# Optimization experiments

Hardware: AMD Instinct MI355X
Metric: run time of the kernel (lower is better)

The kernel has to match this reference:

```python
import jax, jax.numpy as jnp
import numpy as np

DIM = 1024
DFF = 4096
LN_EPS = 1e-5


def _layernorm(x, g, b):
    mu = jnp.mean(x, axis=-1, keepdims=True)
    var = jnp.mean((x - mu) ** 2, axis=-1, keepdims=True)
    return (x - mu) * jax.lax.rsqrt(var + LN_EPS) * g + b


def setup_inputs() -> dict:
    key = jax.random.key(0)
    ks = jax.random.split(key, 16)
    B, L, D, F = 4, 2048, DIM, DFF
    return {
        "x": jax.random.normal(ks[0], (B, L, D), dtype=jnp.float32),
        "hidden_real": jax.random.normal(ks[1], (B, D), dtype=jnp.float32),
        "hidden_imag": jax.random.normal(ks[2], (B, D), dtype=jnp.float32),
        # SConvLayer params (real/imag pairs, mirroring torch.view_as_real storage)
        "phazor_init": jax.random.normal(ks[3], (D, 2), dtype=jnp.float32),
        "phazor": jax.random.normal(ks[4], (D, 2), dtype=jnp.float32),
        # fc (gate) linear
        "fc_w": jax.random.normal(ks[5], (D, D), dtype=jnp.float32) / np.sqrt(D),
        "fc_b": jax.random.normal(ks[6], (D,), dtype=jnp.float32) * 0.01,
        # FFN
        "w1": jax.random.normal(ks[7], (F, D), dtype=jnp.float32) / np.sqrt(D),
        "b1": jax.random.normal(ks[8], (F,), dtype=jnp.float32) * 0.01,
        "w2": jax.random.normal(ks[9], (D, F), dtype=jnp.float32) / np.sqrt(F),
        "b2": jax.random.normal(ks[10], (D,), dtype=jnp.float32) * 0.01,
        # shared LayerNorm (used twice in the block with the same params)
        "ln_g": jnp.ones((D,), dtype=jnp.float32),
        "ln_b": jnp.zeros((D,), dtype=jnp.float32),
    }


def reference(x, hidden_real, hidden_imag, phazor_init, phazor,
              fc_w, fc_b, w1, b1, w2, b2, ln_g, ln_b):
    B, L, D = x.shape
    hidden = (hidden_real + 1j * hidden_imag).astype(jnp.complex64)

    x_res = x
    xn = _layernorm(x, ln_g, ln_b)

    # --- SConvLayer ---
    pz = (phazor[:, 0] + 1j * phazor[:, 1]).astype(jnp.complex64)  # [D]
    # magnitude exp(-|z|^2), phase = angle(z)
    p = jnp.exp(-(pz.real ** 2 + pz.imag ** 2)) * jnp.exp(1j * jnp.angle(pz))
    t = jnp.arange(L)
    prog = p[None, :] ** t[:, None]                      # [L, D] complex
    init_c = (phazor_init[:, 0] + 1j * phazor_init[:, 1]).astype(jnp.complex64)
    filt = prog * init_c[None, :]                        # [L, D]
    n2 = 2 * L
    filt_fft = jnp.fft.fft(filt, n=n2, axis=0)           # [2L, D]
    x_fft = jnp.fft.fft(xn.astype(jnp.complex64), n=n2, axis=1)  # [B, 2L, D]
    conv = jnp.fft.ifft(filt_fft[None] * x_fft, axis=1)[:, :L]   # [B, L, D]
    conv_with_past = conv + hidden[:, None, :] * prog[None] * p[None, None, :]
    sx = conv_with_past.real

    # --- gate ---
    y = jax.nn.silu(jnp.einsum('bld,ed->ble', x_res, fc_w) + fc_b)
    x2 = sx * y + x_res

    # --- FFN (same LayerNorm params) ---
    x3 = _layernorm(x2, ln_g, ln_b)
    h = jax.nn.silu(jnp.einsum('bld,fd->blf', x3, w1) + b1)
    out = jnp.einsum('blf,df->bld', h, w2) + b2 + x2
    return out, conv_with_past
```

## Files before the change

kernel.cpp:

```cpp
#include <hip/hip_runtime.h>
#include <hip/hip_bf16.h>

#define D_MODEL 1024
#define D_FF    4096
#define SEQ_LEN 2048
#define NBATCH  4
#define NROWS   (NBATCH*SEQ_LEN)
#define NCHUNK  32
#define CHUNK_L (SEQ_LEN/NCHUNK)
#define LN_EPS  1e-5f

typedef __hip_bfloat16 bf16;
typedef __attribute__((ext_vector_type(8))) short bf16x8;
typedef __attribute__((ext_vector_type(4))) float f32x4;

__device__ __forceinline__ void gload16(const bf16* g, bf16* l) {
    __builtin_amdgcn_global_load_lds(
        (const __attribute__((address_space(1))) void*)g,
        (__attribute__((address_space(3))) void*)l, 16, 0, 0);
}

__global__ void cast4(const float4* __restrict__ in, ushort4* __restrict__ out, int n4) {
    int i = blockIdx.x * blockDim.x + threadIdx.x;
    if (i < n4) {
        float4 v = in[i];
        union { ushort4 u; bf16 b[4]; } cv;
        cv.b[0] = __float2bfloat16(v.x); cv.b[1] = __float2bfloat16(v.y);
        cv.b[2] = __float2bfloat16(v.z); cv.b[3] = __float2bfloat16(v.w);
        out[i] = cv.u;
    }
}

__global__ void compute_pvec(const float* __restrict__ phz, float* __restrict__ pv) {
    int d = blockIdx.x * blockDim.x + threadIdx.x;
    if (d >= D_MODEL) return;
    float re = phz[2*d], im = phz[2*d+1];
    float r2 = re*re + im*im;
    float mag = expf(-r2);
    float pr, pim;
    if (r2 > 0.f) { float inv = mag / sqrtf(r2); pr = re*inv; pim = im*inv; }
    else          { pr = mag; pim = 0.f; }
    float ar = pr, ai = pim;
    #pragma unroll
    for (int i = 0; i < 6; i++) { float nr = ar*ar - ai*ai; float ni = 2.f*ar*ai; ar = nr; ai = ni; }
    pv[d]            = pr;
    pv[D_MODEL+d]    = pim;
    pv[2*D_MODEL+d]  = ar;
    pv[3*D_MODEL+d]  = ai;
}

__global__ __launch_bounds__(256) void ln_fused(const float* __restrict__ x,
                                                const float* __restrict__ g,
                                                const float* __restrict__ bta,
                                                bf16*  __restrict__ outb,
                                                bf16*  __restrict__ rawb)
{
    int row = blockIdx.x;
    int tid = threadIdx.x;
    const float4* xr = (const float4*)(x + (size_t)row * D_MODEL);
    float4 v = xr[tid];
    if (rawb) {
        union { ushort4 u; bf16 b[4]; } cv;
        cv.b[0]=__float2bfloat16(v.x); cv.b[1]=__float2bfloat16(v.y);
        cv.b[2]=__float2bfloat16(v.z); cv.b[3]=__float2bfloat16(v.w);
        ((ushort4*)(rawb + (size_t)row * D_MODEL))[tid] = cv.u;
    }
    float s  = v.x + v.y + v.z + v.w;
    float s2 = v.x*v.x + v.y*v.y + v.z*v.z + v.w*v.w;
    for (int off = 32; off; off >>= 1) { s += __shfl_down(s, off); s2 += __shfl_down(s2, off); }
    __shared__ float red[8];
    int wid = tid >> 6, lane = tid & 63;
    if (lane == 0) { red[wid] = s; red[4+wid] = s2; }
    __syncthreads();
    if (tid == 0) {
        red[0] = red[0]+red[1]+red[2]+red[3];
        red[4] = red[4]+red[5]+red[6]+red[7];
    }
    __syncthreads();
    float mu  = red[0] * (1.f/D_MODEL);
    float var = red[4] * (1.f/D_MODEL) - mu*mu;
    float rstd = rsqrtf(var + LN_EPS);
    float4 gv = ((const float4*)g)[tid];
    float4 bv = ((const float4*)bta)[tid];
    union { ushort4 u; bf16 b[4]; } cv;
    cv.b[0] = __float2bfloat16((v.x-mu)*rstd*gv.x + bv.x);
    cv.b[1] = __float2bfloat16((v.y-mu)*rstd*gv.y + bv.y);
    cv.b[2] = __float2bfloat16((v.z-mu)*rstd*gv.z + bv.z);
    cv.b[3] = __float2bfloat16((v.w-mu)*rstd*gv.w + bv.w);
    ((ushort4*)(outb + (size_t)row * D_MODEL))[tid] = cv.u;
}

__global__ __launch_bounds__(256) void gate_ln(const float* __restrict__ cwp, int cstride,
                                               const bf16*  __restrict__ y,
                                               const float* __restrict__ x,
                                               const float* __restrict__ g,
                                               const float* __restrict__ bta,
                                               bf16*  __restrict__ x2b,
                                               bf16*  __restrict__ x3b)
{
    int row = blockIdx.x;
    int tid = threadIdx.x;
    size_t base = (size_t)row * D_MODEL + tid*4;
    float4 xv = *(const float4*)(x + base);
    union { ushort4 u; bf16 b[4]; } yv;
    yv.u = *(const ushort4*)(y + base);
    float4 cw;
    if (cstride == 1) {
        cw = *(const float4*)(cwp + base);
    } else {
        const float2* cp = (const float2*)cwp + base;
        cw.x = cp[0].x; cw.y = cp[1].x; cw.z = cp[2].x; cw.w = cp[3].x;
    }
    float4 v;
    v.x = cw.x * __bfloat162float(yv.b[0]) + xv.x;
    v.y = cw.y * __bfloat162float(yv.b[1]) + xv.y;
    v.z = cw.z * __bfloat162float(yv.b[2]) + xv.z;
    v.w = cw.w * __bfloat162float(yv.b[3]) + xv.w;
    union { ushort4 u; bf16 b[4]; } c2;
    c2.b[0]=__float2bfloat16(v.x); c2.b[1]=__float2bfloat16(v.y);
    c2.b[2]=__float2bfloat16(v.z); c2.b[3]=__float2bfloat16(v.w);
    *(ushort4*)(x2b + base) = c2.u;

    float s  = v.x + v.y + v.z + v.w;
    float s2 = v.x*v.x + v.y*v.y + v.z*v.z + v.w*v.w;
    for (int off = 32; off; off >>= 1) { s += __shfl_down(s, off); s2 += __shfl_down(s2, off); }
    __shared__ float red[8];
    int wid = tid >> 6, lane = tid & 63;
    if (lane == 0) { red[wid] = s; red[4+wid] = s2; }
    __syncthreads();
    if (tid == 0) {
        red[0] = red[0]+red[1]+red[2]+red[3];
        red[4] = red[4]+red[5]+red[6]+red[7];
    }
    __syncthreads();
    float mu  = red[0] * (1.f/D_MODEL);
    float var = red[4] * (1.f/D_MODEL) - mu*mu;
    float rstd = rsqrtf(var + LN_EPS);
    float4 gv = ((const float4*)g)[tid];
    float4 bv = ((const float4*)bta)[tid];
    union { ushort4 u; bf16 b[4]; } cv;
    cv.b[0] = __float2bfloat16((v.x-mu)*rstd*gv.x + bv.x);
    cv.b[1] = __float2bfloat16((v.y-mu)*rstd*gv.y + bv.y);
    cv.b[2] = __float2bfloat16((v.z-mu)*rstd*gv.z + bv.z);
    cv.b[3] = __float2bfloat16((v.w-mu)*rstd*gv.w + bv.w);
    *(ushort4*)(x3b + base) = cv.u;
}

__global__ __launch_bounds__(256) void scan_pass1(const bf16* __restrict__ xn,
                                                  const float* __restrict__ pv,
                                                  const float* __restrict__ pini,
                                                  float* __restrict__ Sc)
{
    int d = blockIdx.x * 256 + threadIdx.x;
    int c = blockIdx.y, b = blockIdx.z;
    float pr = pv[d], pim = pv[D_MODEL+d];
    float icr = pini[2*d], ici = pini[2*d+1];
    float Sr = 0.f, Si = 0.f;
    const bf16* xp = xn + ((size_t)b*SEQ_LEN + c*CHUNK_L) * D_MODEL + d;
    #pragma unroll 8
    for (int i = 0; i < CHUNK_L; i++) {
        float xv = __bfloat162float(xp[(size_t)i * D_MODEL]);
        float nr = pr*Sr - pim*Si + icr*xv;
        float ni = pr*Si + pim*Sr + ici*xv;
        Sr = nr; Si = ni;
    }
    size_t o = ((size_t)b*NCHUNK + c) * D_MODEL + d;
    Sc[2*o] = Sr; Sc[2*o+1] = Si;
}

__global__ __launch_bounds__(256) void scan_prefix(const float* __restrict__ Sc,
                                                   const float* __restrict__ pv,
                                                   const float* __restrict__ hr,
                                                   const float* __restrict__ hi,
                                                   float* __restrict__ pref)
{
    int d = blockIdx.x * 256 + threadIdx.x;
    int b = blockIdx.y;
    float qr = pv[2*D_MODEL+d], qi = pv[3*D_MODEL+d];
    float Ur = hr[b*D_MODEL+d], Ui = hi[b*D_MODEL+d];
    for (int c = 0; c < NCHUNK; c++) {
        size_t o = ((size_t)b*NCHUNK + c) * D_MODEL + d;
        pref[2*o] = Ur; pref[2*o+1] = Ui;
        float sr = Sc[2*o], si = Sc[2*o+1];
        float nr = qr*Ur - qi*Ui + sr;
        float ni = qr*Ui + qi*Ur + si;
        Ur = nr; Ui = ni;
    }
}

__global__ __launch_bounds__(256) void scan_pass2(const bf16* __restrict__ xn,
                                                  const float* __restrict__ pv,
                                                  const float* __restrict__ pini,
                                                  const float* __restrict__ pref,
                                                  float* __restrict__ cwp,
                                                  int interleaved)
{
    int d = blockIdx.x * 256 + threadIdx.x;
    int c = blockIdx.y, b = blockIdx.z;
    float pr = pv[d], pim = pv[D_MODEL+d];
    float icr = pini[2*d], ici = pini[2*d+1];
    size_t po = ((size_t)b*NCHUNK + c) * D_MODEL + d;
    float Ur = pref[2*po], Ui = pref[2*po+1];
    size_t base = ((size_t)b*SEQ_LEN + c*CHUNK_L) * D_MODEL + d;
    const bf16* xp = xn + base;
    if (interleaved) {
        float2* cp = (float2*)cwp + base;
        #pragma unroll 8
        for (int i = 0; i < CHUNK_L; i++) {
            float xv = __bfloat162float(xp[(size_t)i * D_MODEL]);
            float nr = pr*Ur - pim*Ui + icr*xv;
            float ni = pr*Ui + pim*Ur + ici*xv;
            Ur = nr; Ui = ni;
            cp[(size_t)i * D_MODEL] = make_float2(Ur, Ui);
        }
    } else {
        float* cp = cwp + base;
        #pragma unroll 8
        for (int i = 0; i < CHUNK_L; i++) {
            float xv = __bfloat162float(xp[(size_t)i * D_MODEL]);
            float nr = pr*Ur - pim*Ui + icr*xv;
            float ni = pr*Ui + pim*Ur + ici*xv;
            Ur = nr; Ui = ni;
            cp[(size_t)i * D_MODEL] = Ur;
        }
    }
}

template<int EPI>
__device__ __forceinline__ void epi_store(float v, size_t idx,
                                          const bf16* e0b, float* outf, bf16* outb)
{
    if (EPI == 1) {
        float yv = v / (1.f + __expf(-v));
        outb[idx] = __float2bfloat16(yv);
    } else {
        outf[idx] = v + __bfloat162float(e0b[idx]);
    }
}

#define BM 128
#define BN 128
#define BK 32

template<int EPI>
__global__ __launch_bounds__(256) void gemm_bt(const bf16* __restrict__ A,
                                               const bf16* __restrict__ Bt,
                                               const float* __restrict__ bias,
                                               const bf16* __restrict__ e0b,
                                               float* __restrict__ outf,
                                               bf16*  __restrict__ outb,
                                               int M, int N, int K)
{
    __shared__ __align__(16) bf16 As[3][BM*BK];
    __shared__ __align__(16) bf16 Bs[3][BM*BK];
    int tid = threadIdx.x;
    int m0 = blockIdx.x * BM;
    int n0 = blockIdx.y * BN;

    int wid = tid >> 6, lane = tid & 63;
    int wm = (wid >> 1) * 64, wn = (wid & 1) * 64;
    int lr = lane & 15;
    int lkc = lane >> 4;

    int rl = lane >> 2;
    int cS = (lane & 3) ^ ((rl >> 1) & 3);
    const bf16* gA0 = A  + (size_t)(m0 +      wid*16 + rl) * K + cS*8;
    const bf16* gA1 = A  + (size_t)(m0 + 64 + wid*16 + rl) * K + cS*8;
    const bf16* gB0 = Bt + (size_t)(n0 +      wid*16 + rl) * K + cS*8;
    const bf16* gB1 = Bt + (size_t)(n0 + 64 + wid*16 + rl) * K + cS*8;
    int lo0 = (     wid*16) * BK;
    int lo1 = (64 + wid*16) * BK;

    int keyr = (lr >> 1) & 3;
    int cR = (lkc ^ keyr) * 8;
    int offA[4], offB[4];
    #pragma unroll
    for (int i = 0; i < 4; i++) {
        offA[i] = (wm + i*16 + lr) * BK + cR;
        offB[i] = (wn + i*16 + lr) * BK + cR;
    }

    int nt = K / BK;
    auto stage = [&](int slot, int tile) {
        int k0 = tile * BK;
        gload16(gA0 + k0, &As[slot][lo0]);
        gload16(gA1 + k0, &As[slot][lo1]);
        gload16(gB0 + k0, &Bs[slot][lo0]);
        gload16(gB1 + k0, &Bs[slot][lo1]);
    };
    f32x4 acc[4][4] = {};
    auto compute = [&](int slot) {
        bf16x8 af[4], bfv[4];
        #pragma unroll
        for (int i = 0; i < 4; i++) {
            af[i]  = *(const bf16x8*)&As[slot][offA[i]];
            bfv[i] = *(const bf16x8*)&Bs[slot][offB[i]];
        }
        #pragma unroll
        for (int i = 0; i < 4; i++)
            #pragma unroll
            for (int j = 0; j < 4; j++)
                acc[i][j] = __builtin_amdgcn_mfma_f32_16x16x32_bf16(af[i], bfv[j], acc[i][j], 0, 0, 0);
    };

    stage(0, 0); stage(1, 1); stage(2, 2);

    int s = 0;
    for (int t = 0; t < nt - 3; ++t) {
        asm volatile("s_waitcnt vmcnt(8)" ::: "memory");
        __builtin_amdgcn_s_barrier();
        __builtin_amdgcn_sched_barrier(0);
        compute(s);
        asm volatile("" ::: "memory");
        __builtin_amdgcn_s_barrier();
        stage(s, t + 3);
        s = (s == 2) ? 0 : s + 1;
    }
    asm volatile("s_waitcnt vmcnt(8)" ::: "memory");
    __builtin_amdgcn_s_barrier();
    __builtin_amdgcn_sched_barrier(0);
    compute(s);
    s = (s == 2) ? 0 : s + 1;
    asm volatile("s_waitcnt vmcnt(4)" ::: "memory");
    __builtin_amdgcn_s_barrier();
    __builtin_amdgcn_sched_barrier(0);
    compute(s);
    s = (s == 2) ? 0 : s + 1;
    asm volatile("s_waitcnt vmcnt(0)" ::: "memory");
    __builtin_amdgcn_s_barrier();
    __builtin_amdgcn_sched_barrier(0);
    compute(s);

    int mrow = 4 * (lane >> 4);
    #pragma unroll
    for (int i = 0; i < 4; i++) {
        #pragma unroll
        for (int j = 0; j < 4; j++) {
            int nb = n0 + wn + j*16 + lr;
            float bb = bias[nb];
            #pragma unroll
            for (int r = 0; r < 4; r++) {
                int m = m0 + wm + i*16 + mrow + r;
                size_t idx = (size_t)m * N + nb;
                epi_store<EPI>(acc[i][j][r] + bb, idx, e0b, outf, outb);
            }
        }
    }
}

#define TM 256
#define TN 256

__global__ __launch_bounds__(512, 2) void gemm256p(const bf16* __restrict__ A,
                                                   const bf16* __restrict__ Bt,
                                                   const float* __restrict__ bias,
                                                   bf16* __restrict__ outb,
                                                   int M, int N, int K)
{
    __shared__ __align__(16) bf16 As[3][TM*BK];
    __shared__ __align__(16) bf16 Bs[3][TN*BK];
    int tid = threadIdx.x;
    int m0 = blockIdx.x * TM;
    int n0 = blockIdx.y * TN;

    int wid = tid >> 6, lane = tid & 63;
    int wr = wid >> 2, wc = wid & 3;
    int wm = wr * 128, wn = wc * 64;
    int lr = lane & 15;
    int lkc = lane >> 4;

    int rs = tid >> 2;
    int cS = (tid & 3) ^ ((rs >> 1) & 3);
    const bf16* gA = A  + (size_t)m0 * K + cS*8;
    const bf16* gB = Bt + (size_t)n0 * K + cS*8;
    int ldst = tid * 8;

    int keyr = (lr >> 1) & 3;
    int cR = (lkc ^ keyr) * 8;
    int offA[8], offB[4];
    #pragma unroll
    for (int i = 0; i < 8; i++) offA[i] = (wm + i*16 + lr) * BK + cR;
    #pragma unroll
    for (int j = 0; j < 4; j++) offB[j] = (wn + j*16 + lr) * BK + cR;

    int nt = K / BK;
    auto stA = [&](int slot, int tile) {
        int k0 = tile * BK;
        gload16(gA + (size_t)rs * K + k0,         &As[slot][ldst]);
        gload16(gA + (size_t)(128 + rs) * K + k0, &As[slot][4096 + ldst]);
    };
    auto stB = [&](int slot, int tile) {
        int k0 = tile * BK;
        gload16(gB + (size_t)rs * K + k0,         &Bs[slot][ldst]);
        gload16(gB + (size_t)(128 + rs) * K + k0, &Bs[slot][4096 + ldst]);
    };

    f32x4 acc[8][4] = {};
    stA(0, 0); stB(0, 0); stA(1, 1); stB(1, 1); stB(2, 2);

    int s = 0;
    for (int t = 0; t < nt; ++t) {
        int sA = (s >= 1) ? s - 1 : 2;
        if (t < nt - 2)       { asm volatile("s_waitcnt vmcnt(6)" ::: "memory"); }
        else if (t == nt - 2) { asm volatile("s_waitcnt vmcnt(4)" ::: "memory"); }
        else                  { asm volatile("s_waitcnt vmcnt(0)" ::: "memory"); }
        __builtin_amdgcn_s_barrier();
        asm volatile("" ::: "memory");
        bf16x8 af0[4], bfv[4];
        #pragma unroll
        for (int i = 0; i < 4; i++) af0[i] = *(const bf16x8*)&As[s][offA[i]];
        #pragma unroll
        for (int j = 0; j < 4; j++) bfv[j] = *(const bf16x8*)&Bs[s][offB[j]];
        if (t + 2 < nt) stA(sA, t + 2);
        asm volatile("s_waitcnt lgkmcnt(0)" ::: "memory");
        __builtin_amdgcn_sched_barrier(0);
        __builtin_amdgcn_s_setprio(1);
        #pragma unroll
        for (int i = 0; i < 4; i++)
            #pragma unroll
            for (int j = 0; j < 4; j++)
                acc[i][j] = __builtin_amdgcn_mfma_f32_16x16x32_bf16(af0[i], bfv[j], acc[i][j], 0, 0, 0);
        __builtin_amdgcn_s_setprio(0);
        __builtin_amdgcn_s_barrier();
        asm volatile("" ::: "memory");
        bf16x8 af1[4];
        #pragma unroll
        for (int i = 0; i < 4; i++) af1[i] = *(const bf16x8*)&As[s][offA[4+i]];
        if (t + 3 < nt) stB(s, t + 3);
        asm volatile("s_waitcnt lgkmcnt(0)" ::: "memory");
        __builtin_amdgcn_sched_barrier(0);
        __builtin_amdgcn_s_setprio(1);
        #pragma unroll
        for (int i = 0; i < 4; i++)
            #pragma unroll
            for (int j = 0; j < 4; j++)
                acc[4+i][j] = __builtin_amdgcn_mfma_f32_16x16x32_bf16(af1[i], bfv[j], acc[4+i][j], 0, 0, 0);
        __builtin_amdgcn_s_setprio(0);
        s = (s == 2) ? 0 : s + 1;
    }
    asm volatile("s_waitcnt vmcnt(0)" ::: "memory");

    int mrow = 4 * (lane >> 4);
    #pragma unroll
    for (int i = 0; i < 8; i++) {
        #pragma unroll
        for (int j = 0; j < 4; j++) {
            int nb = n0 + wn + j*16 + lr;
            float bb = bias[nb];
            #pragma unroll
            for (int r = 0; r < 4; r++) {
                int m = m0 + wm + i*16 + mrow + r;
                size_t idx = (size_t)m * N + nb;
                float v = acc[i][j][r] + bb;
                float yv = v / (1.f + __expf(-v));
                outb[idx] = __float2bfloat16(yv);
            }
        }
    }
}

extern "C" void kernel_launch(void* const* d_in, const int* in_sizes, int n_in,
                              void* d_out, int out_size, void* d_ws, size_t ws_size,
                              hipStream_t stream)
{
    const float* x    = (const float*)d_in[0];
    const float* hr   = (const float*)d_in[1];
    const float* hi   = (const float*)d_in[2];
    const float* pini = (const float*)d_in[3];
    const float* phz  = (const float*)d_in[4];
    const float* fcw  = (const float*)d_in[5];
    const float* fcb  = (const float*)d_in[6];
    const float* w1   = (const float*)d_in[7];
    const float* b1   = (const float*)d_in[8];
    const float* w2   = (const float*)d_in[9];
    const float* b2   = (const float*)d_in[10];
    const float* lng  = (const float*)d_in[11];
    const float* lnb  = (const float*)d_in[12];

    float* out = (float*)d_out;
    float* cwp = out + (size_t)NROWS * D_MODEL;
    int interleaved = (out_size >= NROWS * D_MODEL * 3) ? 1 : 0;

    char* ws = (char*)d_ws;
    size_t off = 0;
    bf16*  wfcb = (bf16*)(ws + off);  off += (size_t)D_MODEL*D_MODEL*2;
    bf16*  w1b  = (bf16*)(ws + off);  off += (size_t)D_FF*D_MODEL*2;
    bf16*  w2b  = (bf16*)(ws + off);  off += (size_t)D_MODEL*D_FF*2;
    float* pv   = (float*)(ws + off); off += (size_t)4*D_MODEL*4;
    bf16*  xnb  = (bf16*)(ws + off);  off += (size_t)NROWS*D_MODEL*2;
    bf16*  xbf  = (bf16*)(ws + off);  off += (size_t)NROWS*D_MODEL*2;
    float* Sc   = (float*)(ws + off); off += (size_t)NBATCH*NCHUNK*D_MODEL*2*4;
    float* pref = (float*)(ws + off); off += (size_t)NBATCH*NCHUNK*D_MODEL*2*4;
    bf16*  x2b  = (bf16*)(ws + off);  off += (size_t)NROWS*D_MODEL*2;
    bf16*  x3b  = (bf16*)(ws + off);  off += (size_t)NROWS*D_MODEL*2;
    bf16*  hbuf = (bf16*)(ws + off);  off += (size_t)NROWS*D_FF*2;
    bf16*  ybuf = (bf16*)(ws + off);  off += (size_t)NROWS*D_MODEL*2;

    cast4<<<1024, 256, 0, stream>>>((const float4*)fcw, (ushort4*)wfcb, D_MODEL*D_MODEL/4);
    cast4<<<4096, 256, 0, stream>>>((const float4*)w1,  (ushort4*)w1b,  D_FF*D_MODEL/4);
    cast4<<<4096, 256, 0, stream>>>((const float4*)w2,  (ushort4*)w2b,  D_MODEL*D_FF/4);

    compute_pvec<<<4, 256, 0, stream>>>(phz, pv);

    ln_fused<<<NROWS, 256, 0, stream>>>(x, lng, lnb, xnb, xbf);

    scan_pass1<<<dim3(4, NCHUNK, NBATCH), 256, 0, stream>>>(xnb, pv, pini, Sc);
    scan_prefix<<<dim3(4, NBATCH), 256, 0, stream>>>(Sc, pv, hr, hi, pref);
    scan_pass2<<<dim3(4, NCHUNK, NBATCH), 256, 0, stream>>>(xnb, pv, pini, pref, cwp, interleaved);

    gemm_bt<1><<<dim3(NROWS/BM, D_MODEL/BN), 256, 0, stream>>>(
        xbf, wfcb, fcb, nullptr, nullptr, ybuf, NROWS, D_MODEL, D_MODEL);

    gate_ln<<<NROWS, 256, 0, stream>>>(cwp, interleaved ? 2 : 1, ybuf, x, lng, lnb, x2b, x3b);

    gemm256p<<<dim3(NROWS/TM, D_FF/TN), 512, 0, stream>>>(
        x3b, w1b, b1, hbuf, NROWS, D_FF, D_MODEL);

    gemm_bt<2><<<dim3(NROWS/BM, D_MODEL/BN), 256, 0, stream>>>(
        hbuf, w2b, b2, x2b, out, nullptr, NROWS, D_MODEL, D_FF);
}
```

Before: 264.1 us.

## Replace 128x128 GEMM with 256x128 tile kernel using split A/B staging

Replaces the 128x128 tiled GEMM used for the gate and FFN down-projection with a 256x128 tile kernel, where each wave computes a 128x64 sub-tile in two halves. A and B tile loads are staged separately and interleaved between the two MFMA halves, with s_setprio raised around the MFMA blocks. The larger M tile is meant to raise arithmetic intensity per LDS/global load. In exchange it doubles the accumulator registers, which may lower occupancy, and halves the grid to 256 blocks.

New measurement: 289.3 us. +9.6%, slower.

```diff
diff --git a/kernel.cpp b/kernel.cpp
--- a/kernel.cpp
+++ b/kernel.cpp
@@ -226,114 +226,108 @@
     }
 }
 
+#define BK 32
+
+#define TMN_M 256
+#define TMN_N 128
+
 template<int EPI>
-__device__ __forceinline__ void epi_store(float v, size_t idx,
-                                          const bf16* e0b, float* outf, bf16* outb)
-{
-    if (EPI == 1) {
-        float yv = v / (1.f + __expf(-v));
-        outb[idx] = __float2bfloat16(yv);
-    } else {
-        outf[idx] = v + __bfloat162float(e0b[idx]);
-    }
-}
-
-#define BM 128
-#define BN 128
-#define BK 32
-
-template<int EPI>
-__global__ __launch_bounds__(256) void gemm_bt(const bf16* __restrict__ A,
-                                               const bf16* __restrict__ Bt,
-                                               const float* __restrict__ bias,
-                                               const bf16* __restrict__ e0b,
-                                               float* __restrict__ outf,
-                                               bf16*  __restrict__ outb,
-                                               int M, int N, int K)
-{
-    __shared__ __align__(16) bf16 As[3][BM*BK];
-    __shared__ __align__(16) bf16 Bs[3][BM*BK];
+__global__ __launch_bounds__(256) void gemm256n(const bf16* __restrict__ A,
+                                                const bf16* __restrict__ Bt,
+                                                const float* __restrict__ bias,
+                                                const bf16* __restrict__ e0b,
+                                                float* __restrict__ outf,
+                                                bf16*  __restrict__ outb,
+                                                int M, int N, int K)
+{
+    __shared__ __align__(16) bf16 As[3][TMN_M*BK];
+    __shared__ __align__(16) bf16 Bs[3][TMN_N*BK];
     int tid = threadIdx.x;
-    int m0 = blockIdx.x * BM;
-    int n0 = blockIdx.y * BN;
+    int m0 = blockIdx.x * TMN_M;
+    int n0 = blockIdx.y * TMN_N;
 
     int wid = tid >> 6, lane = tid & 63;
-    int wm = (wid >> 1) * 64, wn = (wid & 1) * 64;
+    int wr = wid >> 1, wc = wid & 1;
+    int wm = wr * 128, wn = wc * 64;
     int lr = lane & 15;
     int lkc = lane >> 4;
 
-    int rl = lane >> 2;
-    int cS = (lane & 3) ^ ((rl >> 1) & 3);
-    const bf16* gA0 = A  + (size_t)(m0 +      wid*16 + rl) * K + cS*8;
-    const bf16* gA1 = A  + (size_t)(m0 + 64 + wid*16 + rl) * K + cS*8;
-    const bf16* gB0 = Bt + (size_t)(n0 +      wid*16 + rl) * K + cS*8;
-    const bf16* gB1 = Bt + (size_t)(n0 + 64 + wid*16 + rl) * K + cS*8;
-    int lo0 = (     wid*16) * BK;
-    int lo1 = (64 + wid*16) * BK;
+    int rs = tid >> 2;
+    int cS = (tid & 3) ^ ((rs >> 1) & 3);
+    const bf16* gA = A  + (size_t)m0 * K + cS*8;
+    const bf16* gB = Bt + (size_t)n0 * K + cS*8;
+    int ldst = tid * 8;
 
     int keyr = (lr >> 1) & 3;
     int cR = (lkc ^ keyr) * 8;
-    int offA[4], offB[4];
-    #pragma unroll
-    for (int i = 0; i < 4; i++) {
-        offA[i] = (wm + i*16 + lr) * BK + cR;
-        offB[i] = (wn + i*16 + lr) * BK + cR;
-    }
+    int offA[8], offB[4];
+    #pragma unroll
+    for (int i = 0; i < 8; i++) offA[i] = (wm + i*16 + lr) * BK + cR;
+    #pragma unroll
+    for (int j = 0; j < 4; j++) offB[j] = (wn + j*16 + lr) * BK + cR;
 
     int nt = K / BK;
-    auto stage = [&](int slot, int tile) {
+    auto stA = [&](int slot, int tile) {
         int k0 = tile * BK;
-        gload16(gA0 + k0, &As[slot][lo0]);
-        gload16(gA1 + k0, &As[slot][lo1]);
-        gload16(gB0 + k0, &Bs[slot][lo0]);
-        gload16(gB1 + k0, &Bs[slot][lo1]);
+        #pragma unroll
+        for (int g = 0; g < 4; g++)
+            gload16(gA + (size_t)(g*64 + rs) * K + k0, &As[slot][g*2048 + ldst]);
     };
-    f32x4 acc[4][4] = {};
-    auto compute = [&](int slot) {
-        bf16x8 af[4], bfv[4];
-        #pragma unroll
-        for (int i = 0; i < 4; i++) {
-            af[i]  = *(const bf16x8*)&As[slot][offA[i]];
-            bfv[i] = *(const bf16x8*)&Bs[slot][offB[i]];
-        }
+    auto stB = [&](int slot, int tile) {
+        int k0 = tile * BK;
+        #pragma unroll
+        for (int g = 0; g < 2; g++)
+            gload16(gB + (size_t)(g*64 + rs) * K + k0, &Bs[slot][g*2048 + ldst]);
+    };
+
+    f32x4 acc[8][4] = {};
+    stA(0, 0); stB(0, 0); stA(1, 1); stB(1, 1); stB(2, 2);
+
+    int s = 0;
+    for (int t = 0; t < nt; ++t) {
+        int sA = (s >= 1) ? s - 1 : 2;
+        if (t < nt - 2)       { asm volatile("s_waitcnt vmcnt(8)" ::: "memory"); }
+        else if (t == nt - 2) { asm volatile("s_waitcnt vmcnt(6)" ::: "memory"); }
+        else                  { asm volatile("s_waitcnt vmcnt(0)" ::: "memory"); }
+        __builtin_amdgcn_s_barrier();
+        asm volatile("" ::: "memory");
+        bf16x8 af0[4], bfv[4];
+        #pragma unroll
+        for (int i = 0; i < 4; i++) af0[i] = *(const bf16x8*)&As[s][offA[i]];
+        #pragma unroll
+        for (int j = 0; j < 4; j++) bfv[j] = *(const bf16x8*)&Bs[s][offB[j]];
+        if (t + 2 < nt) stA(sA, t + 2);
+        asm volatile("s_waitcnt lgkmcnt(0)" ::: "memory");
+        __builtin_amdgcn_sched_barrier(0);
+        __builtin_amdgcn_s_setprio(1);
         #pragma unroll
         for (int i = 0; i < 4; i++)
             #pragma unroll
             for (int j = 0; j < 4; j++)
-                acc[i][j] = __builtin_amdgcn_mfma_f32_16x16x32_bf16(af[i], bfv[j], acc[i][j], 0, 0, 0);
-    };
-
-    stage(0, 0); stage(1, 1); stage(2, 2);
-
-    int s = 0;
-    for (int t = 0; t < nt - 3; ++t) {
-        asm volatile("s_waitcnt vmcnt(8)" ::: "memory");
+                acc[i][j] = __builtin_amdgcn_mfma_f32_16x16x32_bf16(af0[i], bfv[j], acc[i][j], 0, 0, 0);
+        __builtin_amdgcn_s_setprio(0);
         __builtin_amdgcn_s_barrier();
+        asm volatile("" ::: "memory");
+        bf16x8 af1[4];
+        #pragma unroll
+        for (int i = 0; i < 4; i++) af1[i] = *(const bf16x8*)&As[s][offA[4+i]];
+        if (t + 3 < nt) stB(s, t + 3);
+        asm volatile("s_waitcnt lgkmcnt(0)" ::: "memory");
         __builtin_amdgcn_sched_barrier(0);
-        compute(s);
-        asm volatile("" ::: "memory");
-        __builtin_amdgcn_s_barrier();
-        stage(s, t + 3);
+        __builtin_amdgcn_s_setprio(1);
+        #pragma unroll
+        for (int i = 0; i < 4; i++)
+            #pragma unroll
+            for (int j = 0; j < 4; j++)
+                acc[4+i][j] = __builtin_amdgcn_mfma_f32_16x16x32_bf16(af1[i], bfv[j], acc[4+i][j], 0, 0, 0);
+        __builtin_amdgcn_s_setprio(0);
         s = (s == 2) ? 0 : s + 1;
     }
-    asm volatile("s_waitcnt vmcnt(8)" ::: "memory");
-    __builtin_amdgcn_s_barrier();
-    __builtin_amdgcn_sched_barrier(0);
-    compute(s);
-    s = (s == 2) ? 0 : s + 1;
-    asm volatile("s_waitcnt vmcnt(4)" ::: "memory");
-    __builtin_amdgcn_s_barrier();
-    __builtin_amdgcn_sched_barrier(0);
-    compute(s);
-    s = (s == 2) ? 0 : s + 1;
     asm volatile("s_waitcnt vmcnt(0)" ::: "memory");
-    __builtin_amdgcn_s_barrier();
-    __builtin_amdgcn_sched_barrier(0);
-    compute(s);
 
     int mrow = 4 * (lane >> 4);
     #pragma unroll
-    for (int i = 0; i < 4; i++) {
+    for (int i = 0; i < 8; i++) {
         #pragma unroll
         for (int j = 0; j < 4; j++) {
             int nb = n0 + wn + j*16 + lr;
@@ -342,7 +336,13 @@
             for (int r = 0; r < 4; r++) {
                 int m = m0 + wm + i*16 + mrow + r;
                 size_t idx = (size_t)m * N + nb;
-                epi_store<EPI>(acc[i][j][r] + bb, idx, e0b, outf, outb);
+                float v = acc[i][j][r] + bb;
+                if (EPI == 1) {
+                    float yv = v / (1.f + __expf(-v));
+                    outb[idx] = __float2bfloat16(yv);
+                } else {
+                    outf[idx] = v + __bfloat162float(e0b[idx]);
+                }
             }
         }
     }
@@ -508,7 +508,7 @@
     scan_prefix<<<dim3(4, NBATCH), 256, 0, stream>>>(Sc, pv, hr, hi, pref);
     scan_pass2<<<dim3(4, NCHUNK, NBATCH), 256, 0, stream>>>(xnb, pv, pini, pref, cwp, interleaved);
 
-    gemm_bt<1><<<dim3(NROWS/BM, D_MODEL/BN), 256, 0, stream>>>(
+    gemm256n<1><<<dim3(NROWS/TMN_M, D_MODEL/TMN_N), 256, 0, stream>>>(
         xbf, wfcb, fcb, nullptr, nullptr, ybuf, NROWS, D_MODEL, D_MODEL);
 
     gate_ln<<<NROWS, 256, 0, stream>>>(cwp, interleaved ? 2 : 1, ybuf, x, lng, lnb, x2b, x3b);
@@ -516,6 +516,6 @@
     gemm256p<<<dim3(NROWS/TM, D_FF/TN), 512, 0, stream>>>(
         x3b, w1b, b1, hbuf, NROWS, D_FF, D_MODEL);
 
-    gemm_bt<2><<<dim3(NROWS/BM, D_MODEL/BN), 256, 0, stream>>>(
+    gemm256n<2><<<dim3(NROWS/TMN_M, D_MODEL/TMN_N), 256, 0, stream>>>(
         hbuf, w2b, b2, x2b, out, nullptr, NROWS, D_MODEL, D_FF);
 }
```
